# Kernel optimization log

Hardware: AMD Instinct MI355X
Metric: run time of the kernel (lower is better)

Reference implementation:

```python
import jax, jax.numpy as jnp
import numpy as np
import math

B, T, C, H = 4, 2048, 1024, 16
D = C // H  # head dim = 64

def setup_inputs() -> dict:
    key = jax.random.key(0)
    k1, k2, k3 = jax.random.split(key, 3)
    scale = 0.02
    return {
        "x": jax.random.normal(k1, (B, T, C), dtype=jnp.float32),
        "W_qkv": jax.random.normal(k2, (C, 3 * C), dtype=jnp.float32) * scale,
        "b_qkv": jnp.zeros((3 * C,), dtype=jnp.float32),
        "W_proj": jax.random.normal(k3, (C, C), dtype=jnp.float32) * scale,
        "b_proj": jnp.zeros((C,), dtype=jnp.float32),
    }

def reference(x, W_qkv, b_qkv, W_proj, b_proj):
    Bx, Tx, Cx = x.shape
    qkv = x @ W_qkv + b_qkv                      # [B, T, 3C]
    q, k, v = jnp.split(qkv, 3, axis=-1)
    # [B, T, C] -> [B, H, T, D]
    q = q.reshape(Bx, Tx, H, D).transpose(0, 2, 1, 3)
    k = k.reshape(Bx, Tx, H, D).transpose(0, 2, 1, 3)
    v = v.reshape(Bx, Tx, H, D).transpose(0, 2, 1, 3)
    scores = jnp.einsum("bhqd,bhkd->bhqk", q, k) * (1.0 / math.sqrt(D))
    causal = jnp.tril(jnp.ones((Tx, Tx), dtype=bool))  # [T, T]
    scores = jnp.where(causal[None, None, :, :], scores, jnp.finfo(scores.dtype).min)
    attn = jax.nn.softmax(scores, axis=-1)
    # dropout(p=0.1) in the original is stochastic; omitted for a deterministic baseline
    out = jnp.einsum("bhqk,bhkd->bhqd", attn, v)   # [B, H, T, D]
    out = out.transpose(0, 2, 1, 3).reshape(Bx, Tx, Cx)
    return out @ W_proj + b_proj
```

## Files before the change

kernel.cpp:

```cpp
#include <hip/hip_runtime.h>
#include <hip/hip_bf16.h>
#include <cstdint>
#include <cstddef>

#define Bsz 4
#define Tseq 2048
#define Cdim 1024
#define Hh 16
#define Dh 64

typedef unsigned short u16;
typedef __bf16 bfx8 __attribute__((ext_vector_type(8)));
typedef float f32x4 __attribute__((ext_vector_type(4)));
typedef float f32x16 __attribute__((ext_vector_type(16)));
typedef unsigned short u16x8 __attribute__((ext_vector_type(8)));

#define AS1 __attribute__((address_space(1)))
#define AS3 __attribute__((address_space(3)))

#define QSCALE 0.18033688f

__device__ __forceinline__ u16 f2b(float f) {
  union { float f; unsigned u; } x; x.f = f;
  unsigned r = x.u + 0x7FFFu + ((x.u >> 16) & 1u);
  return (u16)(r >> 16);
}
__device__ __forceinline__ float b2f(u16 b) {
  union { unsigned u; float f; } x; x.u = ((unsigned)b) << 16; return x.f;
}
__device__ __forceinline__ unsigned cvtpk(float lo, float hi) {
  unsigned r;
  asm("v_cvt_pk_bf16_f32 %0, %1, %2" : "=v"(r) : "v"(lo), "v"(hi));
  return r;
}
__device__ __forceinline__ void swap32(unsigned &a, unsigned &b) {
  asm("v_permlane32_swap_b32 %0, %1" : "+v"(a), "+v"(b));
}

__global__ __launch_bounds__(256) void cvt_f32_bf16(const float* __restrict__ in,
                                                    u16* __restrict__ out, int n4) {
  int i = blockIdx.x * 256 + threadIdx.x;
  if (i < n4) {
    const float4 v = reinterpret_cast<const float4*>(in)[i];
    ushort4 o;
    o.x = f2b(v.x); o.y = f2b(v.y); o.z = f2b(v.z); o.w = f2b(v.w);
    reinterpret_cast<ushort4*>(out)[i] = o;
  }
}

__global__ __launch_bounds__(256) void transpose_cvt(const float* __restrict__ in,
                                                     u16* __restrict__ out, int R, int Cn) {
  __shared__ float tile[32][33];
  const int c0 = blockIdx.x * 32, r0 = blockIdx.y * 32;
  const int tx = threadIdx.x, ty = threadIdx.y;
  for (int i = ty; i < 32; i += 8)
    tile[i][tx] = in[(size_t)(r0 + i) * Cn + c0 + tx];
  __syncthreads();
  for (int i = ty; i < 32; i += 8)
    out[(size_t)(c0 + i) * R + r0 + tx] = f2b(tile[tx][i]);
}

template<int MODE>
__global__ __launch_bounds__(256) void gemm_bt(const u16* __restrict__ A, const u16* __restrict__ Bt,
                                               const float* __restrict__ bias, void* __restrict__ Cout,
                                               u16* __restrict__ vtout,
                                               int M, int N, int K) {
  __shared__ __align__(16) u16 Alds[128 * 32];
  __shared__ __align__(16) u16 Blds[128 * 32];
  const int tid = threadIdx.x;
  const int lane = tid & 63;
  const int wid = tid >> 6;
  const int nwgx = gridDim.x;
  const int nwg = nwgx * gridDim.y;
  int lin = blockIdx.y * nwgx + blockIdx.x;
  lin = (lin & 7) * (nwg >> 3) + (lin >> 3);
  const int mbase = (lin / nwgx) * 128;
  const int nbase = (lin % nwgx) * 128;
  const int wm = wid & 1, wn = wid >> 1;

  const f32x4 vzero = {0.f, 0.f, 0.f, 0.f};
  f32x4 acc[4][4];
  #pragma unroll
  for (int i = 0; i < 4; ++i)
    #pragma unroll
    for (int j = 0; j < 4; ++j) acc[i][j] = vzero;

  const int sr = lane >> 2;
  const int sc = (lane & 3) * 8;

  for (int k0 = 0; k0 < K; k0 += 32) {
    __syncthreads();
    #pragma unroll
    for (int c = 0; c < 2; ++c) {
      const int chunk = wid * 2 + c;
      const u16* ga = A  + (size_t)(mbase + chunk * 16 + sr) * K + k0 + sc;
      const u16* gb = Bt + (size_t)(nbase + chunk * 16 + sr) * K + k0 + sc;
      __builtin_amdgcn_global_load_lds((AS1 void*)const_cast<u16*>(ga),
                                       (AS3 void*)&Alds[chunk * 512], 16, 0, 0);
      __builtin_amdgcn_global_load_lds((AS1 void*)const_cast<u16*>(gb),
                                       (AS3 void*)&Blds[chunk * 512], 16, 0, 0);
    }
    __syncthreads();

    bfx8 af[4], bfr[4];
    #pragma unroll
    for (int mf = 0; mf < 4; ++mf)
      af[mf] = *reinterpret_cast<const bfx8*>(&Alds[(wm * 64 + mf * 16 + (lane & 15)) * 32 + (lane >> 4) * 8]);
    #pragma unroll
    for (int nf = 0; nf < 4; ++nf)
      bfr[nf] = *reinterpret_cast<const bfx8*>(&Blds[(wn * 64 + nf * 16 + (lane & 15)) * 32 + (lane >> 4) * 8]);
    __builtin_amdgcn_s_setprio(1);
    #pragma unroll
    for (int mf = 0; mf < 4; ++mf)
      #pragma unroll
      for (int nf = 0; nf < 4; ++nf)
        acc[mf][nf] = __builtin_amdgcn_mfma_f32_16x16x32_bf16(af[mf], bfr[nf], acc[mf][nf], 0, 0, 0);
    __builtin_amdgcn_s_setprio(0);
  }

  float bv[4];
  #pragma unroll
  for (int nf = 0; nf < 4; ++nf) bv[nf] = bias[nbase + wn * 64 + nf * 16 + (lane & 15)];
  #pragma unroll
  for (int mf = 0; mf < 4; ++mf) {
    #pragma unroll
    for (int nf = 0; nf < 4; ++nf) {
      const int r0 = mbase + wm * 64 + mf * 16 + (lane >> 4) * 4;
      const int c  = nbase + wn * 64 + nf * 16 + (lane & 15);
      const int cb = nbase + wn * 64 + nf * 16;
      const float cscale = (MODE == 1 && cb >= 1024 && cb < 2048) ? QSCALE : 1.0f;
      float v[4];
      #pragma unroll
      for (int j = 0; j < 4; ++j) v[j] = (acc[mf][nf][j] + bv[nf]) * cscale;
      if (MODE == 1 && cb >= 2048) {
        const int hh = (c - 2048) >> 6, dd = (c - 2048) & 63;
        const int bb = r0 >> 11, tt = r0 & 2047;
        ushort4 pkd;
        pkd.x = f2b(v[0]); pkd.y = f2b(v[1]); pkd.z = f2b(v[2]); pkd.w = f2b(v[3]);
        *reinterpret_cast<ushort4*>(
            &vtout[(((size_t)bb * Hh + hh) * Dh + dd) * Tseq + tt]) = pkd;
      } else {
        #pragma unroll
        for (int j = 0; j < 4; ++j) {
          if (MODE == 1) ((u16*)Cout)[(size_t)(r0 + j) * N + c] = f2b(v[j]);
          else           ((float*)Cout)[(size_t)(r0 + j) * N + c] = v[j];
        }
      }
    }
  }
}

#define ROWI(r) (((r) & 3) + 8 * ((r) >> 2))
__global__ __launch_bounds__(512, 4) void attn_fwd(const u16* __restrict__ qkv,
                                                   const u16* __restrict__ vt,
                                                   u16* __restrict__ aout) {
  __shared__ __align__(16) u16 Klds[4][64 * 64];
  __shared__ __align__(16) u16 Vtlds[4][64 * 64];
  const int tid = threadIdx.x;
  const int lane = tid & 63;
  const int wid = tid >> 6;
  const int qg = wid & 3;
  const int half = wid >> 2;
  const int lin = blockIdx.y * gridDim.x + blockIdx.x;
  const int bh = (lin & 7) * 8 + ((lin >> 3) & 7);
  const int qpair = lin >> 6;
  const int b = bh >> 4, h = bh & 15;
  const int hi4 = (lane & 32) >> 3;

  const int stg_row = lane >> 3;
  const int stg_srcslot = (lane & 7) ^ (stg_row & 7);

  const u16* gkbase = qkv + ((size_t)b * Tseq + wid * 8 + stg_row) * 3072
                      + 1024 + h * 64 + stg_srcslot * 8;
  const u16* gvbase = vt + ((size_t)bh * Dh + wid * 8 + stg_row) * Tseq + stg_srcslot * 8;

  float* Olds = reinterpret_cast<float*>(&Klds[0][0]);
  float* Llds = reinterpret_cast<float*>(&Vtlds[0][0]);

  #pragma unroll 1
  for (int pass = 0; pass < 2; ++pass) {
    const int qtile = pass ? qpair : (15 - qpair);
    const int qwb = qtile * 128 + qg * 32;
    const int ntiles = qtile * 2 + 2;

    bfx8 qf[4];
    {
      const int qrow = qwb + (lane & 31);
      #pragma unroll
      for (int c = 0; c < 4; ++c) {
        const u16* src = qkv + (size_t)(b * Tseq + qrow) * 3072 + h * 64 + c * 16 + (hi4 << 1);
        qf[c] = *reinterpret_cast<const bfx8*>(src);
      }
    }

    float l_r = 0.f;
    f32x16 o0, o1;
    #pragma unroll
    for (int r = 0; r < 16; ++r) { o0[r] = 0.f; o1[r] = 0.f; }

    auto stageT = [&](int t) {
      const u16* gk = gkbase + (size_t)t * 64 * 3072;
      const u16* gv = gvbase + t * 64;
      __builtin_amdgcn_global_load_lds((AS1 void*)const_cast<u16*>(gk),
                                       (AS3 void*)&Klds[t & 3][wid * 512], 16, 0, 0);
      __builtin_amdgcn_global_load_lds((AS1 void*)const_cast<u16*>(gv),
                                       (AS3 void*)&Vtlds[t & 3][wid * 512], 16, 0, 0);
    };
    stageT(0);
    stageT(1);
    __syncthreads();

    for (int t = 0; t < ntiles; t += 2) {
      if (t + 2 < ntiles) stageT(t + 2);
      if (t + 3 < ntiles) stageT(t + 3);

      const int tt = t + half;
      const int kb = tt * 64;
      const int buf = tt & 3;
      if (kb <= qwb + 31) {
        f32x16 st0, st1;
        #pragma unroll
        for (int r = 0; r < 16; ++r) { st0[r] = 0.f; st1[r] = 0.f; }
        __builtin_amdgcn_s_setprio(1);
        #pragma unroll
        for (int c = 0; c < 4; ++c) {
          const int row0 = lane & 31;
          const int sl = (c * 2 + (lane >> 5)) ^ (row0 & 7);
          const bfx8 k0 = *reinterpret_cast<const bfx8*>(&Klds[buf][row0 * 64 + sl * 8]);
          const bfx8 k1 = *reinterpret_cast<const bfx8*>(&Klds[buf][(row0 + 32) * 64 + sl * 8]);
          st0 = __builtin_amdgcn_mfma_f32_32x32x16_bf16(k0, qf[c], st0, 0, 0, 0);
          st1 = __builtin_amdgcn_mfma_f32_32x32x16_bf16(k1, qf[c], st1, 0, 0, 0);
        }
        __builtin_amdgcn_s_setprio(0);

        if (kb + 63 > qwb) {
          const int qg_ = qwb + (lane & 31);
          #pragma unroll
          for (int r = 0; r < 16; ++r) {
            const int kt = kb + ROWI(r) + hi4;
            if (kt > qg_) st0[r] = -1e30f;
            if (kt + 32 > qg_) st1[r] = -1e30f;
          }
        }

        float rs = 0.f;
        #pragma unroll
        for (int r = 0; r < 16; ++r) { st0[r] = exp2f(st0[r]); rs += st0[r]; }
        #pragma unroll
        for (int r = 0; r < 16; ++r) { st1[r] = exp2f(st1[r]); rs += st1[r]; }
        rs += __shfl_xor(rs, 32);
        l_r += rs;

        bfx8 pf[4];
        #pragma unroll
        for (int tph = 0; tph < 2; ++tph) {
          #pragma unroll
          for (int c2 = 0; c2 < 2; ++c2) {
            const int rb = c2 * 8;
            float s0 = tph ? st1[rb + 0] : st0[rb + 0], s1 = tph ? st1[rb + 1] : st0[rb + 1];
            float s2 = tph ? st1[rb + 2] : st0[rb + 2], s3 = tph ? st1[rb + 3] : st0[rb + 3];
            float s4 = tph ? st1[rb + 4] : st0[rb + 4], s5 = tph ? st1[rb + 5] : st0[rb + 5];
            float s6 = tph ? st1[rb + 6] : st0[rb + 6], s7 = tph ? st1[rb + 7] : st0[rb + 7];
            unsigned w0 = cvtpk(s0, s1);
            unsigned w2 = cvtpk(s4, s5);
            swap32(w0, w2);
            unsigned w1 = cvtpk(s2, s3);
            unsigned w3 = cvtpk(s6, s7);
            swap32(w1, w3);
            union { unsigned w[4]; bfx8 v; } u;
            u.w[0] = w0; u.w[1] = w1; u.w[2] = w2; u.w[3] = w3;
            pf[tph * 2 + c2] = u.v;
          }
        }

        __builtin_amdgcn_s_setprio(1);
        #pragma unroll
        for (int c4 = 0; c4 < 4; ++c4) {
          const int vrow = lane & 31;
          const int sl = (c4 * 2 + (lane >> 5)) ^ (vrow & 7);
          const bfx8 vf0 = *reinterpret_cast<const bfx8*>(&Vtlds[buf][vrow * 64 + sl * 8]);
          const bfx8 vf1 = *reinterpret_cast<const bfx8*>(&Vtlds[buf][(vrow + 32) * 64 + sl * 8]);
          o0 = __builtin_amdgcn_mfma_f32_32x32x16_bf16(pf[c4], vf0, o0, 0, 0, 0);
          o1 = __builtin_amdgcn_mfma_f32_32x32x16_bf16(pf[c4], vf1, o1, 0, 0, 0);
        }
        __builtin_amdgcn_s_setprio(0);
      }

      __syncthreads();
    }

    if (half == 1) {
      Llds[qg * 64 + lane] = l_r;
      #pragma unroll
      for (int r = 0; r < 16; ++r) {
        Olds[qg * 2048 + r * 64 + lane]        = o0[r];
        Olds[qg * 2048 + (r + 16) * 64 + lane] = o1[r];
      }
    }
    __syncthreads();
    if (half == 0) {
      const float l1 = Llds[qg * 64 + lane];
      const float linv = 1.0f / (l_r + l1);
      #pragma unroll
      for (int r = 0; r < 16; ++r) {
        const int src = ROWI(r) + hi4;
        const float cr = __shfl(linv, src);
        const int q = qwb + src;
        const float v0 = (o0[r] + Olds[qg * 2048 + r * 64 + lane]) * cr;
        const float v1 = (o1[r] + Olds[qg * 2048 + (r + 16) * 64 + lane]) * cr;
        aout[(size_t)(b * Tseq + q) * 1024 + h * 64 + (lane & 31)]      = f2b(v0);
        aout[(size_t)(b * Tseq + q) * 1024 + h * 64 + 32 + (lane & 31)] = f2b(v1);
      }
    }
    __syncthreads();
  }
}

extern "C" void kernel_launch(void* const* d_in, const int* in_sizes, int n_in,
                              void* d_out, int out_size, void* d_ws, size_t ws_size,
                              hipStream_t stream) {
  const float* x      = (const float*)d_in[0];
  const float* W_qkv  = (const float*)d_in[1];
  const float* b_qkv  = (const float*)d_in[2];
  const float* W_proj = (const float*)d_in[3];
  const float* b_proj = (const float*)d_in[4];
  float* out = (float*)d_out;

  char* ws = (char*)d_ws;
  const size_t SZ_XB    = 16777216;
  const size_t SZ_WQKV  = 6291456;
  const size_t SZ_WPROJ = 2097152;
  const size_t SZ_QKV   = 50331648;
  u16* xb     = (u16*)ws;
  u16* wqkvT  = (u16*)(ws + SZ_XB);
  u16* wprojT = (u16*)(ws + SZ_XB + SZ_WQKV);
  u16* qkv    = (u16*)(ws + SZ_XB + SZ_WQKV + SZ_WPROJ);
  u16* vt     = (u16*)(ws + SZ_XB + SZ_WQKV + SZ_WPROJ + SZ_QKV);

  cvt_f32_bf16<<<dim3((Bsz * Tseq * Cdim / 4 + 255) / 256), dim3(256), 0, stream>>>(
      x, xb, Bsz * Tseq * Cdim / 4);
  transpose_cvt<<<dim3(3 * Cdim / 32, Cdim / 32), dim3(32, 8), 0, stream>>>(W_qkv, wqkvT, Cdim, 3 * Cdim);
  transpose_cvt<<<dim3(Cdim / 32, Cdim / 32), dim3(32, 8), 0, stream>>>(W_proj, wprojT, Cdim, Cdim);
  gemm_bt<1><<<dim3(3 * Cdim / 128, Bsz * Tseq / 128), dim3(256), 0, stream>>>(
      xb, wqkvT, b_qkv, qkv, vt, Bsz * Tseq, 3 * Cdim, Cdim);
  attn_fwd<<<dim3(8, Bsz * Hh), dim3(512), 0, stream>>>(qkv, vt, xb);
  gemm_bt<0><<<dim3(Cdim / 128, Bsz * Tseq / 128), dim3(256), 0, stream>>>(
      xb, wprojT, b_proj, out, nullptr, Bsz * Tseq, Cdim, Cdim);
}
```

Baseline: 180.0 us.

## Triple-buffer GEMM LDS staging with swizzled layout and 128x256 tiles

Rewrites the bf16 GEMM main loop to use a three-slot LDS ring, prefetching two K-steps ahead with global_load_lds. This replaces the two-barrier-per-step load-then-compute pattern with a single barrier and partial vmcnt waits. The tile grows to 128x256 with 512 threads (8 waves), and an XOR swizzle on LDS rows is meant to cut bank conflicts for ds_read_b128. In exchange it uses more LDS per block and hand-written asm waitcnt logic, which can limit occupancy and is fragile if the count of outstanding loads changes.

```diff
diff --git a/kernel.cpp b/kernel.cpp
--- a/kernel.cpp
+++ b/kernel.cpp
@@ -61,12 +61,12 @@
 }
 
 template<int MODE>
-__global__ __launch_bounds__(256) void gemm_bt(const u16* __restrict__ A, const u16* __restrict__ Bt,
-                                               const float* __restrict__ bias, void* __restrict__ Cout,
-                                               u16* __restrict__ vtout,
-                                               int M, int N, int K) {
-  __shared__ __align__(16) u16 Alds[128 * 32];
-  __shared__ __align__(16) u16 Blds[128 * 32];
+__global__ __launch_bounds__(512, 4) void gemm_bt(const u16* __restrict__ A, const u16* __restrict__ Bt,
+                                                  const float* __restrict__ bias, void* __restrict__ Cout,
+                                                  u16* __restrict__ vtout,
+                                                  int M, int N, int K) {
+  __shared__ __align__(16) u16 Alds[3][4096];
+  __shared__ __align__(16) u16 Blds[3][8192];
   const int tid = threadIdx.x;
   const int lane = tid & 63;
   const int wid = tid >> 6;
@@ -75,8 +75,29 @@
   int lin = blockIdx.y * nwgx + blockIdx.x;
   lin = (lin & 7) * (nwg >> 3) + (lin >> 3);
   const int mbase = (lin / nwgx) * 128;
-  const int nbase = (lin % nwgx) * 128;
+  const int nbase = (lin % nwgx) * 256;
   const int wm = wid & 1, wn = wid >> 1;
+
+  const int sLlow = lane >> 3;
+  const int s8 = (lane & 7) ^ sLlow;
+  const int srow = 2 * (wid * 8 + sLlow) + (s8 >> 2);
+  const int skof = (s8 & 3) * 8;
+
+  const u16* pa  = A  + (size_t)(mbase + srow) * K + skof;
+  const u16* pb0 = Bt + (size_t)(nbase + srow) * K + skof;
+  const u16* pb1 = pb0 + (size_t)128 * K;
+
+  const int raA = wm * 64 + (lane & 15);
+  const int LA = raA >> 1;
+  const int pA = ((raA & 1) * 4 + (lane >> 4)) ^ (LA & 7);
+  const int aoffw = LA * 64 + pA * 8;
+  const int rbB = wn * 64 + (lane & 15);
+  const int LB = rbB >> 1;
+  const int pB = ((rbB & 1) * 4 + (lane >> 4)) ^ (LB & 7);
+  const int boffw = LB * 64 + pB * 8;
+
+  AS3 u16* aldsb = (AS3 u16*)&Alds[0][0];
+  AS3 u16* bldsb = (AS3 u16*)&Blds[0][0];
 
   const f32x4 vzero = {0.f, 0.f, 0.f, 0.f};
   f32x4 acc[4][4];
@@ -85,37 +106,57 @@
     #pragma unroll
     for (int j = 0; j < 4; ++j) acc[i][j] = vzero;
 
-  const int sr = lane >> 2;
-  const int sc = (lane & 3) * 8;
-
-  for (int k0 = 0; k0 < K; k0 += 32) {
-    __syncthreads();
-    #pragma unroll
-    for (int c = 0; c < 2; ++c) {
-      const int chunk = wid * 2 + c;
-      const u16* ga = A  + (size_t)(mbase + chunk * 16 + sr) * K + k0 + sc;
-      const u16* gb = Bt + (size_t)(nbase + chunk * 16 + sr) * K + k0 + sc;
-      __builtin_amdgcn_global_load_lds((AS1 void*)const_cast<u16*>(ga),
-                                       (AS3 void*)&Alds[chunk * 512], 16, 0, 0);
-      __builtin_amdgcn_global_load_lds((AS1 void*)const_cast<u16*>(gb),
-                                       (AS3 void*)&Blds[chunk * 512], 16, 0, 0);
-    }
-    __syncthreads();
-
-    bfx8 af[4], bfr[4];
-    #pragma unroll
-    for (int mf = 0; mf < 4; ++mf)
-      af[mf] = *reinterpret_cast<const bfx8*>(&Alds[(wm * 64 + mf * 16 + (lane & 15)) * 32 + (lane >> 4) * 8]);
-    #pragma unroll
-    for (int nf = 0; nf < 4; ++nf)
-      bfr[nf] = *reinterpret_cast<const bfx8*>(&Blds[(wn * 64 + nf * 16 + (lane & 15)) * 32 + (lane >> 4) * 8]);
+  const int NT = K >> 5;
+
+  auto stage = [&](int slot) {
+    __builtin_amdgcn_global_load_lds((AS1 void*)const_cast<u16*>(pa),
+                                     (AS3 void*)&Alds[slot][wid * 512], 16, 0, 0);
+    __builtin_amdgcn_global_load_lds((AS1 void*)const_cast<u16*>(pb0),
+                                     (AS3 void*)&Blds[slot][wid * 512], 16, 0, 0);
+    __builtin_amdgcn_global_load_lds((AS1 void*)const_cast<u16*>(pb1),
+                                     (AS3 void*)&Blds[slot][4096 + wid * 512], 16, 0, 0);
+    pa += 32; pb0 += 32; pb1 += 32;
+  };
+
+  stage(0);
+  stage(1);
+  asm volatile("s_waitcnt vmcnt(3)" ::: "memory");
+  __builtin_amdgcn_s_barrier();
+
+  int slot = 0, pf = 2;
+  for (int t = 0; t < NT; ++t) {
+    if (t + 2 < NT) stage(pf);
+
+    bfx8 af[4], bfv[4];
+    {
+      AS3 u16* ap = aldsb + slot * 4096 + aoffw;
+      AS3 u16* bp = bldsb + slot * 8192 + boffw;
+      asm volatile("ds_read_b128 %0, %1"             : "=v"(af[0])  : "v"(ap));
+      asm volatile("ds_read_b128 %0, %1 offset:1024" : "=v"(af[1])  : "v"(ap));
+      asm volatile("ds_read_b128 %0, %1 offset:2048" : "=v"(af[2])  : "v"(ap));
+      asm volatile("ds_read_b128 %0, %1 offset:3072" : "=v"(af[3])  : "v"(ap));
+      asm volatile("ds_read_b128 %0, %1"             : "=v"(bfv[0]) : "v"(bp));
+      asm volatile("ds_read_b128 %0, %1 offset:1024" : "=v"(bfv[1]) : "v"(bp));
+      asm volatile("ds_read_b128 %0, %1 offset:2048" : "=v"(bfv[2]) : "v"(bp));
+      asm volatile("ds_read_b128 %0, %1 offset:3072" : "=v"(bfv[3]) : "v"(bp));
+    }
+    asm volatile("s_waitcnt lgkmcnt(0)" ::: "memory");
+    __builtin_amdgcn_sched_barrier(0);
+
     __builtin_amdgcn_s_setprio(1);
     #pragma unroll
     for (int mf = 0; mf < 4; ++mf)
       #pragma unroll
       for (int nf = 0; nf < 4; ++nf)
-        acc[mf][nf] = __builtin_amdgcn_mfma_f32_16x16x32_bf16(af[mf], bfr[nf], acc[mf][nf], 0, 0, 0);
+        acc[mf][nf] = __builtin_amdgcn_mfma_f32_16x16x32_bf16(af[mf], bfv[nf], acc[mf][nf], 0, 0, 0);
     __builtin_amdgcn_s_setprio(0);
+
+    if (t + 2 < NT)      { asm volatile("s_waitcnt vmcnt(3)" ::: "memory"); }
+    else if (t + 1 < NT) { asm volatile("s_waitcnt vmcnt(0)" ::: "memory"); }
+    if (t + 1 < NT) __builtin_amdgcn_s_barrier();
+
+    slot = (slot == 2) ? 0 : slot + 1;
+    pf   = (pf == 2) ? 0 : pf + 1;
   }
 
   float bv[4];
@@ -341,9 +382,9 @@
       x, xb, Bsz * Tseq * Cdim / 4);
   transpose_cvt<<<dim3(3 * Cdim / 32, Cdim / 32), dim3(32, 8), 0, stream>>>(W_qkv, wqkvT, Cdim, 3 * Cdim);
   transpose_cvt<<<dim3(Cdim / 32, Cdim / 32), dim3(32, 8), 0, stream>>>(W_proj, wprojT, Cdim, Cdim);
-  gemm_bt<1><<<dim3(3 * Cdim / 128, Bsz * Tseq / 128), dim3(256), 0, stream>>>(
+  gemm_bt<1><<<dim3(3 * Cdim / 256, Bsz * Tseq / 128), dim3(512), 0, stream>>>(
       xb, wqkvT, b_qkv, qkv, vt, Bsz * Tseq, 3 * Cdim, Cdim);
   attn_fwd<<<dim3(8, Bsz * Hh), dim3(512), 0, stream>>>(qkv, vt, xb);
-  gemm_bt<0><<<dim3(Cdim / 128, Bsz * Tseq / 128), dim3(256), 0, stream>>>(
+  gemm_bt<0><<<dim3(Cdim / 256, Bsz * Tseq / 128), dim3(512), 0, stream>>>(
       xb, wprojT, b_proj, out, nullptr, Bsz * Tseq, Cdim, Cdim);
 }
```

Result: faster. 167.4 us (-7.0%).
